# Performance work log

Hardware: AMD Instinct MI355X
Metric: run time of the kernel (lower is better)

## Reference

```python
import jax, jax.numpy as jnp
import numpy as np

B, N, C, D, E, VOC, T = 128, 49, 2048, 512, 512, 10000, 20


def setup_inputs() -> dict:
    key = jax.random.key(0)
    ks = jax.random.split(key, 24)
    rn = lambda k, s: (jax.random.normal(k, s) * 0.02).astype(jnp.float32)
    z = lambda s: jnp.zeros(s, dtype=jnp.float32)
    return {
        "image_feature": jax.random.normal(ks[0], (B, N, C), dtype=jnp.float32),
        "target": jax.random.randint(ks[1], (B, T), 0, VOC),
        "emb": rn(ks[2], (VOC, E)),
        "Wa": rn(ks[3], (D, C)), "ba": z((D,)),
        "Wb": rn(ks[4], (D, C)), "bb": z((D,)),
        "Whi": rn(ks[5], (D, C)), "bhi": z((D,)),
        "Wmi": rn(ks[6], (D, C)), "bmi": z((D,)),
        "Wih": rn(ks[7], (4 * D, D + E)), "bih": z((4 * D,)),
        "Whh": rn(ks[8], (4 * D, D)), "bhh": z((4 * D,)),
        "Wv": rn(ks[9], (N, D)),
        "Wg": rn(ks[10], (N, D)),
        "wh": rn(ks[11], (1, N)),
        "WH": rn(ks[12], (D, D)),
        "Wx": rn(ks[13], (D, D + E)),
        "Wh2": rn(ks[14], (D, D)),
        "Ws": rn(ks[15], (N, D)),
        "Wc": rn(ks[16], (D, D)), "bc": z((D,)),
        "Wfc": rn(ks[17], (D, D)), "bfc": z((D,)),
        "Wp": rn(ks[18], (VOC, D)), "bp": z((VOC,)),
    }


def _forward(image_feature, target, emb, Wa, ba, Wb, bb, Whi, bhi, Wmi, bmi,
             Wih, bih, Whh, bhh, Wv, Wg, wh, WH, Wx, Wh2, Ws, Wc, bc,
             Wfc, bfc, Wp, bp):
    relu, sig = jax.nn.relu, jax.nn.sigmoid
    Vf = relu(jnp.einsum('bnc,dc->bnd', image_feature, Wa) + ba)  # [B,N,D]
    mean = image_feature.mean(axis=1)                             # [B,C]
    vg = relu(mean @ Wb.T + bb)                                   # [B,D]
    h0 = relu(mean @ Whi.T + bhi)
    m0 = relu(mean @ Wmi.T + bmi)
    zbase = jnp.einsum('bnd,kd->bnk', Vf, Wv)                     # [B,N,N], fixed per image

    we = emb[target]                                              # [B,T,E]
    we = jnp.concatenate([jnp.zeros((we.shape[0], 1, we.shape[2]), we.dtype), we[:, :-1]], axis=1)
    we_t = jnp.swapaxes(we, 0, 1)                                 # [T,B,E]

    def step(carry, wemb):
        h, m = carry
        x = jnp.concatenate([vg, wemb], axis=1)                   # [B,D+E]
        hp = h
        gates = x @ Wih.T + bih + h @ Whh.T + bhh
        i, f, g, o = jnp.split(gates, 4, axis=1)
        m2 = sig(f) * m + sig(i) * jnp.tanh(g)
        h2 = sig(o) * jnp.tanh(m2)
        H = relu(h2 @ WH.T)                                       # [B,D]
        gH = H @ Wg.T                                             # [B,N]
        z = jnp.squeeze(jnp.tanh(zbase + gH[:, None, :]) @ wh.T, -1)  # [B,N]
        gt = sig(x @ Wx.T + hp @ Wh2.T)                           # [B,D]
        s = relu((gt * jnp.tanh(m2)) @ Wc.T + bc)                 # [B,D]
        z2 = jnp.tanh(s @ Ws.T + gH) @ wh.T                       # [B,1]
        alpha = jax.nn.softmax(jnp.concatenate([z, z2], axis=1), axis=1)  # [B,N+1]
        ctx = jnp.einsum('bn,bnd->bd', alpha[:, :-1], Vf) + alpha[:, -1:] * s
        out = jnp.tanh((H + ctx) @ Wfc.T + bfc)
        logit = out @ Wp.T + bp                                   # [B,VOC]
        return (h2, m2), (logit, alpha[:, :-1])

    _, (logits, attn) = jax.lax.scan(step, (h0, m0), we_t)
    logits = jnp.swapaxes(logits, 0, 1)                           # [B,T,VOC]
    attn = jnp.swapaxes(attn, 0, 1)                               # [B,T,N]
    return jax.nn.log_softmax(logits, axis=2), attn


def reference(image_feature, target, emb, Wa, ba, Wb, bb, Whi, bhi, Wmi, bmi,
              Wih, bih, Whh, bhh, Wv, Wg, wh, WH, Wx, Wh2, Ws, Wc, bc,
              Wfc, bfc, Wp, bp):
    return _forward(image_feature, target, emb, Wa, ba, Wb, bb, Whi, bhi,
                    Wmi, bmi, Wih, bih, Whh, bhh, Wv, Wg, wh, WH, Wx, Wh2,
                    Ws, Wc, bc, Wfc, bfc, Wp, bp)
```

## Files before the change

kernel.cpp:

```cpp
#include <hip/hip_runtime.h>
#include <hip/hip_bf16.h>

static const int kB = 128, kN = 49, kC = 2048, kD = 512, kE = 512, kV = 10000, kT = 20;

typedef __bf16 bf16x8 __attribute__((ext_vector_type(8)));
typedef float  f32x4v __attribute__((ext_vector_type(4)));
typedef _Float16 h8_t __attribute__((ext_vector_type(8)));
typedef _Float16 h2v_t __attribute__((ext_vector_type(2)));
typedef unsigned short u16;
typedef unsigned int u32;

#if defined(__has_builtin)
#if __has_builtin(__builtin_amdgcn_fdot2)
#define HAS_FDOT2 1
#endif
#endif
#ifndef HAS_FDOT2
#define HAS_FDOT2 0
#endif

#define AS1 __attribute__((address_space(1)))
#define AS3 __attribute__((address_space(3)))

__device__ __forceinline__ float sigmoidf_(float x){ return 1.f/(1.f+expf(-x)); }
__device__ __forceinline__ u16 f2b(float x){ __hip_bfloat16 h = __float2bfloat16(x); return *(u16*)&h; }
__device__ __forceinline__ float bu2f(u32 u){ u32 w = u << 16; union{u32 u; float f;} c; c.u = w; return c.f; }

#define TBM 128
#define TBN 128
#define TBK 32

__global__ __launch_bounds__(256) void gemm_bf16(
    const u16* __restrict__ A, int lda,
    const u16* __restrict__ W, int ldw,
    float* __restrict__ C, u16* __restrict__ Cbf, int ldc,
    int M, int N, int K,
    const float* __restrict__ bias,
    const float* __restrict__ add1, int ld1, int a1mask,
    int act,
    const u16* __restrict__ mul2, int ldm,
    int swz)
{
    __shared__ __align__(16) u16 As[TBM*TBK];
    __shared__ __align__(16) u16 Bs[TBN*TBK];
    const int tid = threadIdx.x;
    int bm, bn;
    if (swz){
        const int mblocks = (M + TBM - 1)/TBM;
        const int per_g = mblocks*8;
        const int id = blockIdx.x;
        const int g = id/per_g, r = id - g*per_g;
        bm = (r >> 3)*TBM;
        bn = (g*8 + (r & 7))*TBN;
        if (bn >= N) return;
    } else {
        bm = blockIdx.y * TBM;
        bn = blockIdx.x * TBN;
    }
    const int wave = tid >> 6, lane = tid & 63;
    const int wm = (wave >> 1) * 64, wn = (wave & 1) * 64;
    const int lm = lane & 15, quad = lane >> 4;
    f32x4v acc[4][4] = {};
    for (int k0 = 0; k0 < K; k0 += TBK) {
        #pragma unroll
        for (int h = 0; h < 2; ++h) {
            const int slot = h*256 + tid;
            const int row = slot >> 2, kf = (slot & 3)*8;
            const int wbase = (h*256 + (tid & 448))*8;
            __builtin_amdgcn_global_load_lds((const AS1 u32*)(A + (size_t)(bm + row)*lda + k0 + kf),
                                             (AS3 u32*)(As + wbase), 16, 0, 0);
            __builtin_amdgcn_global_load_lds((const AS1 u32*)(W + (size_t)(bn + row)*ldw + k0 + kf),
                                             (AS3 u32*)(Bs + wbase), 16, 0, 0);
        }
        __syncthreads();
        bf16x8 afr[4], bfr[4];
        #pragma unroll
        for (int i = 0; i < 4; ++i) afr[i] = *(const bf16x8*)&As[(wm + i*16 + lm)*TBK + quad*8];
        #pragma unroll
        for (int j = 0; j < 4; ++j) bfr[j] = *(const bf16x8*)&Bs[(wn + j*16 + lm)*TBK + quad*8];
        #pragma unroll
        for (int i = 0; i < 4; ++i)
            #pragma unroll
            for (int j = 0; j < 4; ++j)
                acc[i][j] = __builtin_amdgcn_mfma_f32_16x16x32_bf16(afr[i], bfr[j], acc[i][j], 0, 0, 0);
        __syncthreads();
    }
    #pragma unroll
    for (int i = 0; i < 4; ++i) {
        int mbase = bm + wm + i*16 + quad*4;
        #pragma unroll
        for (int j = 0; j < 4; ++j) {
            int n = bn + wn + j*16 + lm;
            if (n >= N) continue;
            float bv = bias ? bias[n] : 0.f;
            #pragma unroll
            for (int rr2 = 0; rr2 < 4; ++rr2) {
                int m = mbase + rr2;
                float v = acc[i][j][rr2] + bv;
                if (add1) v += add1[(size_t)(m & a1mask)*ld1 + n];
                if (act == 1) v = fmaxf(v, 0.f);
                else if (act == 2) v = tanhf(v);
                else if (act == 3) v = sigmoidf_(v) * bu2f(mul2[(size_t)m*ldm + n]);
                if (C)   C[(size_t)m*ldc + n] = v;
                if (Cbf) Cbf[(size_t)m*ldc + n] = f2b(v);
            }
        }
    }
}

__global__ __launch_bounds__(256) void img_cvt_mean_k(const float* __restrict__ img,
                                                      u16* __restrict__ img_bf,
                                                      u16* __restrict__ meanb){
    int idx = blockIdx.x*256 + threadIdx.x;
    int b = idx >> 8, c8 = idx & 255;
    const float* p = img + (size_t)b*kN*kC + c8*8;
    f32x4v s0 = {0,0,0,0}, s1 = {0,0,0,0};
    for (int n = 0; n < kN; ++n){
        f32x4v f0 = *(const f32x4v*)(p + (size_t)n*kC);
        f32x4v f1 = *(const f32x4v*)(p + (size_t)n*kC + 4);
        s0 += f0; s1 += f1;
        union { u16 u[8]; uint4 v; } pk;
        pk.u[0]=f2b(f0[0]); pk.u[1]=f2b(f0[1]); pk.u[2]=f2b(f0[2]); pk.u[3]=f2b(f0[3]);
        pk.u[4]=f2b(f1[0]); pk.u[5]=f2b(f1[1]); pk.u[6]=f2b(f1[2]); pk.u[7]=f2b(f1[3]);
        *(uint4*)(img_bf + ((size_t)(b*kN + n))*kC + c8*8) = pk.v;
    }
    const float inv = 1.f/(float)kN;
    union { u16 u[8]; uint4 v; } pm;
    pm.u[0]=f2b(s0[0]*inv); pm.u[1]=f2b(s0[1]*inv); pm.u[2]=f2b(s0[2]*inv); pm.u[3]=f2b(s0[3]*inv);
    pm.u[4]=f2b(s1[0]*inv); pm.u[5]=f2b(s1[1]*inv); pm.u[6]=f2b(s1[2]*inv); pm.u[7]=f2b(s1[3]*inv);
    *(uint4*)(meanb + (size_t)b*kC + c8*8) = pm.v;
}

struct CvtDesc {
    const float* src;
    unsigned long long dst;
    int src_ld, Kshift, mode, start;
};
struct CvtTab { CvtDesc d[17]; int total; };

__global__ __launch_bounds__(256) void multi_cvt_k(CvtTab tab){
    for (int idx = blockIdx.x*256 + threadIdx.x; idx < tab.total; idx += gridDim.x*256){
        int di = 0;
        #pragma unroll
        for (int i = 1; i < 17; ++i) if (idx >= tab.d[i].start) di = i;
        const CvtDesc D = tab.d[di];
        int rel = idx - D.start;
        int rr = rel >> D.Kshift, kc = rel - (rr << D.Kshift);
        const float* p = D.src + (size_t)rr*D.src_ld + kc*8;
        f32x4v f0 = *(const f32x4v*)p, f1 = *(const f32x4v*)(p+4);
        if (D.mode == 0){
            union { u16 u[8]; uint4 v; } pk;
            pk.u[0]=f2b(f0[0]); pk.u[1]=f2b(f0[1]); pk.u[2]=f2b(f0[2]); pk.u[3]=f2b(f0[3]);
            pk.u[4]=f2b(f1[0]); pk.u[5]=f2b(f1[1]); pk.u[6]=f2b(f1[2]); pk.u[7]=f2b(f1[3]);
            *(uint4*)((u16*)D.dst + (((size_t)rr << D.Kshift) + kc)*8) = pk.v;
        } else {
            h8_t o;
            o[0]=(_Float16)f0[0]; o[1]=(_Float16)f0[1]; o[2]=(_Float16)f0[2]; o[3]=(_Float16)f0[3];
            o[4]=(_Float16)f1[0]; o[5]=(_Float16)f1[1]; o[6]=(_Float16)f1[2]; o[7]=(_Float16)f1[3];
            *(h8_t*)((_Float16*)D.dst + ((size_t)kc*2048 + rr)*8) = o;
        }
    }
}

__global__ __launch_bounds__(256) void bias_prep_k(const float* bih, const float* bhh,
                                                   const float* bb, const float* bhi, const float* bmi,
                                                   float* bias2560, float* bcat3){
    int i = blockIdx.x*256 + threadIdx.x;
    if (i < 2048) bias2560[i] = bih[i] + bhh[i];
    else if (i < 2560) bias2560[i] = 0.f;
    else if (i < 4096){
        int j = i - 2560;
        bcat3[j] = (j < 512) ? bb[j] : (j < 1024 ? bhi[j-512] : bmi[j-1024]);
    }
}

__global__ __launch_bounds__(256) void emb_gather_k(const int* __restrict__ target,
                                                    const float* __restrict__ emb,
                                                    u16* __restrict__ we){
    int idx = blockIdx.x*256 + threadIdx.x;
    int e = idx & (kE-1);
    int rr = idx >> 9;
    int b = rr & 127, t = rr >> 7;
    float v = 0.f;
    if (t > 0){ int tok = target[b*kT + (t-1)]; v = emb[(size_t)tok*kE + e]; }
    we[idx] = f2b(v);
}

__global__ __launch_bounds__(256) void initcopy_k(const float* __restrict__ initC,
                                                  u16* __restrict__ hp_bf){
    int idx = blockIdx.x*256 + threadIdx.x;
    int b = idx >> 9, d = idx & 511;
    hp_bf[idx] = f2b(initC[(size_t)b*1536 + 512 + d]);
}

__device__ __forceinline__ float dot8f(h8_t a, h8_t b, float c){
#if HAS_FDOT2
    const h2v_t* ap = (const h2v_t*)&a;
    const h2v_t* bp = (const h2v_t*)&b;
    c = __builtin_amdgcn_fdot2(ap[0], bp[0], c, false);
    c = __builtin_amdgcn_fdot2(ap[1], bp[1], c, false);
    c = __builtin_amdgcn_fdot2(ap[2], bp[2], c, false);
    c = __builtin_amdgcn_fdot2(ap[3], bp[3], c, false);
#else
    #pragma unroll
    for (int i = 0; i < 8; ++i) c = fmaf((float)a[i], (float)b[i], c);
#endif
    return c;
}

__global__ __launch_bounds__(1024, 1) void scan_k(
    const float* __restrict__ initC,
    const float* __restrict__ xall,
    const _Float16* __restrict__ Wrec,
    u16* __restrict__ hp_bf,
    u16* __restrict__ tm_bf)
{
    const int b = blockIdx.x, tid = threadIdx.x;
    const int out = tid & 511, kh = tid >> 9;
    __shared__ __align__(16) _Float16 sh[512];
    __shared__ float spart[512][4];

    if (tid < 512) sh[tid] = (_Float16)initC[(size_t)b*1536 + 512 + tid];
    float m_reg = (kh == 0) ? initC[(size_t)b*1536 + 1024 + out] : 0.f;
    __syncthreads();

    for (int t = 0; t < kT; ++t){
        float a0=0.f, a1=0.f, a2=0.f, a3=0.f;
        const int kc0 = kh*32;
        #pragma unroll 2
        for (int kc = kc0; kc < kc0 + 32; ++kc){
            h8_t hv = *(const h8_t*)&sh[kc*8];
            const _Float16* wb = Wrec + (size_t)kc*2048*8;
            a0 = dot8f(hv, *(const h8_t*)&wb[(size_t)(out       )*8], a0);
            a1 = dot8f(hv, *(const h8_t*)&wb[(size_t)(out +  512)*8], a1);
            a2 = dot8f(hv, *(const h8_t*)&wb[(size_t)(out + 1024)*8], a2);
            a3 = dot8f(hv, *(const h8_t*)&wb[(size_t)(out + 1536)*8], a3);
        }
        __syncthreads();
        if (kh == 1){
            spart[out][0]=a0; spart[out][1]=a1; spart[out][2]=a2; spart[out][3]=a3;
        }
        __syncthreads();
        if (kh == 0){
            const float* xrow = xall + ((size_t)t*kB + b)*2560;
            a0 += spart[out][0] + xrow[out];
            a1 += spart[out][1] + xrow[out + 512];
            a2 += spart[out][2] + xrow[out + 1024];
            a3 += spart[out][3] + xrow[out + 1536];
            float i_g = sigmoidf_(a0), f_g = sigmoidf_(a1);
            float g_g = tanhf(a2),     o_g = sigmoidf_(a3);
            m_reg = f_g*m_reg + i_g*g_g;
            float tm = tanhf(m_reg);
            float h2 = o_g*tm;
            sh[out] = (_Float16)h2;
            hp_bf[((size_t)(t+1)*kB + b)*512 + out] = f2b(h2);
            tm_bf[((size_t)t*kB + b)*512 + out] = f2b(tm);
        }
        __syncthreads();
    }
}

__global__ __launch_bounds__(256) void attn_k(
    const float* __restrict__ H_all,
    const float* __restrict__ s_all,
    const u16* __restrict__ Wg_bf,
    const u16* __restrict__ Ws_bf,
    const u16* __restrict__ Vf_bf,
    const float* __restrict__ zbase,
    const float* __restrict__ wh,
    u16* __restrict__ Hc_bf,
    float* __restrict__ attn_out)
{
    const int r = blockIdx.x, tid = threadIdx.x;
    const int b = r & 127, t = r >> 7;
    __shared__ float sH2[512], ss2[512];
    __shared__ float sgH[52], ssWs[52], swh[52], sz[52], salpha[52];

    for (int d = tid; d < 512; d += 256){
        sH2[d] = H_all[(size_t)r*512 + d];
        ss2[d] = s_all[(size_t)r*512 + d];
    }
    if (tid < 49) swh[tid] = wh[tid];
    __syncthreads();
    if (tid < 49){
        const u16* wr = Wg_bf + (size_t)tid*512;
        float a = 0.f;
        for (int k = 0; k < 512; k += 8){
            uint4 v = *(const uint4*)(wr + k);
            a += bu2f(v.x&0xffff)*sH2[k]   + bu2f(v.x>>16)*sH2[k+1]
               + bu2f(v.y&0xffff)*sH2[k+2] + bu2f(v.y>>16)*sH2[k+3]
               + bu2f(v.z&0xffff)*sH2[k+4] + bu2f(v.z>>16)*sH2[k+5]
               + bu2f(v.w&0xffff)*sH2[k+6] + bu2f(v.w>>16)*sH2[k+7];
        }
        sgH[tid] = a;
    } else if (tid >= 64 && tid < 113){
        int n = tid - 64;
        const u16* wr = Ws_bf + (size_t)n*512;
        float a = 0.f;
        for (int k = 0; k < 512; k += 8){
            uint4 v = *(const uint4*)(wr + k);
            a += bu2f(v.x&0xffff)*ss2[k]   + bu2f(v.x>>16)*ss2[k+1]
               + bu2f(v.y&0xffff)*ss2[k+2] + bu2f(v.y>>16)*ss2[k+3]
               + bu2f(v.z&0xffff)*ss2[k+4] + bu2f(v.z>>16)*ss2[k+5]
               + bu2f(v.w&0xffff)*ss2[k+6] + bu2f(v.w>>16)*ss2[k+7];
        }
        ssWs[n] = a;
    }
    __syncthreads();
    if (tid < 49){
        const float* zb = zbase + (size_t)b*2401 + (size_t)tid*49;
        float a = 0.f;
        #pragma unroll
        for (int k = 0; k < 49; ++k) a += tanhf(zb[k] + sgH[k]) * swh[k];
        sz[tid] = a;
    } else if (tid == 64){
        float a = 0.f;
        #pragma unroll
        for (int k = 0; k < 49; ++k) a += tanhf(ssWs[k] + sgH[k]) * swh[k];
        sz[49] = a;
    }
    __syncthreads();
    if (tid < 64){
        float val = (tid < 50) ? sz[tid] : -1e30f;
        float mx = val;
        #pragma unroll
        for (int o = 32; o > 0; o >>= 1) mx = fmaxf(mx, __shfl_xor(mx, o));
        float e = (tid < 50) ? __expf(val - mx) : 0.f;
        float ssum = e;
        #pragma unroll
        for (int o = 32; o > 0; o >>= 1) ssum += __shfl_xor(ssum, o);
        float a = e/ssum;
        if (tid < 50) salpha[tid] = a;
        if (tid < 49) attn_out[((size_t)b*kT + t)*kN + tid] = a;
    }
    __syncthreads();
    for (int d = tid; d < 512; d += 256){
        float a = salpha[49] * ss2[d];
        const u16* vf = Vf_bf + (size_t)b*49*512 + d;
        #pragma unroll
        for (int n = 0; n < 49; ++n) a = fmaf(salpha[n], bu2f(vf[(size_t)n*512]), a);
        Hc_bf[(size_t)r*512 + d] = f2b(sH2[d] + a);
    }
}

__global__ __launch_bounds__(256) void logsoftmax_k(const u16* __restrict__ logits_bf,
                                                    float* __restrict__ out0)
{
    const int r = blockIdx.x, tid = threadIdx.x;
    const int b = r / 20, t = r - b*20;
    const u16* L = logits_bf + (size_t)(t*kB + b)*kV;
    __shared__ float rm[256], rs[256];
    float m = -1e30f, s = 0.f;
    for (int c = tid; c < kV/8; c += 256){
        uint4 v = *(const uint4*)(L + c*8);
        u32 w[4] = {v.x, v.y, v.z, v.w};
        #pragma unroll
        for (int j = 0; j < 4; ++j){
            float x0 = bu2f(w[j] & 0xffff), x1 = bu2f(w[j] >> 16);
            float nm = fmaxf(m, fmaxf(x0, x1));
            s = s*__expf(m - nm) + __expf(x0 - nm) + __expf(x1 - nm);
            m = nm;
        }
    }
    rm[tid] = m; rs[tid] = s; __syncthreads();
    for (int st = 128; st > 0; st >>= 1){
        if (tid < st){
            float m2 = rm[tid + st], s2 = rs[tid + st];
            float nm = fmaxf(rm[tid], m2);
            rs[tid] = rs[tid]*__expf(rm[tid] - nm) + s2*__expf(m2 - nm);
            rm[tid] = nm;
        }
        __syncthreads();
    }
    float lse = rm[0] + logf(rs[0]);
    float* D = out0 + (size_t)r*kV;
    for (int c = tid; c < kV/8; c += 256){
        uint4 v = *(const uint4*)(L + c*8);
        u32 w[4] = {v.x, v.y, v.z, v.w};
        f32x4v o0, o1;
        o0[0]=bu2f(w[0]&0xffff)-lse; o0[1]=bu2f(w[0]>>16)-lse;
        o0[2]=bu2f(w[1]&0xffff)-lse; o0[3]=bu2f(w[1]>>16)-lse;
        o1[0]=bu2f(w[2]&0xffff)-lse; o1[1]=bu2f(w[2]>>16)-lse;
        o1[2]=bu2f(w[3]&0xffff)-lse; o1[3]=bu2f(w[3]>>16)-lse;
        *(f32x4v*)(D + c*8) = o0;
        *(f32x4v*)(D + c*8 + 4) = o1;
    }
}

extern "C" void kernel_launch(void* const* d_in, const int* in_sizes, int n_in,
                              void* d_out, int out_size, void* d_ws, size_t ws_size,
                              hipStream_t stream)
{
    const float* img   = (const float*)d_in[0];
    const int*   target= (const int*)  d_in[1];
    const float* emb   = (const float*)d_in[2];
    const float* Wa    = (const float*)d_in[3];
    const float* ba    = (const float*)d_in[4];
    const float* Wb    = (const float*)d_in[5];
    const float* bb    = (const float*)d_in[6];
    const float* Whi   = (const float*)d_in[7];
    const float* bhi   = (const float*)d_in[8];
    const float* Wmi   = (const float*)d_in[9];
    const float* bmi   = (const float*)d_in[10];
    const float* Wih   = (const float*)d_in[11];
    const float* bih   = (const float*)d_in[12];
    const float* Whh   = (const float*)d_in[13];
    const float* bhh   = (const float*)d_in[14];
    const float* Wv    = (const float*)d_in[15];
    const float* Wg    = (const float*)d_in[16];
    const float* wh    = (const float*)d_in[17];
    const float* W_H   = (const float*)d_in[18];
    const float* Wx    = (const float*)d_in[19];
    const float* Wh2   = (const float*)d_in[20];
    const float* Wsm   = (const float*)d_in[21];
    const float* Wc    = (const float*)d_in[22];
    const float* bc    = (const float*)d_in[23];
    const float* Wfc   = (const float*)d_in[24];
    const float* bfc   = (const float*)d_in[25];
    const float* Wp    = (const float*)d_in[26];
    const float* bp    = (const float*)d_in[27];
    (void)in_sizes; (void)n_in; (void)out_size; (void)ws_size;

    float* out0 = (float*)d_out;
    float* attn_out = out0 + (size_t)kB*kT*kV;

    char* base = (char*)d_ws;
    size_t off = 0;
    auto alloc = [&](size_t bytes)->char*{
        char* p = base + off;
        off += ((bytes + 255) & ~(size_t)255);
        return p;
    };
    u16* Wa_bf     = (u16*)alloc((size_t)kD*kC*2);
    u16* Winit_bf  = (u16*)alloc((size_t)1536*kC*2);
    u16* Wv_bf     = (u16*)alloc((size_t)128*kD*2);
    u16* Wp_bf     = (u16*)alloc((size_t)10112*kD*2);
    u16* Wfirst_bf = (u16*)alloc((size_t)2560*512*2);
    u16* Wlast_bf  = (u16*)alloc((size_t)2560*512*2);
    _Float16* Wrec4 = (_Float16*)alloc((size_t)2048*512*2);
    u16* Wh2_bf    = (u16*)alloc((size_t)512*512*2);
    u16* WH_bf     = (u16*)alloc((size_t)512*512*2);
    u16* Wc_bf     = (u16*)alloc((size_t)512*512*2);
    u16* Wg_bf     = (u16*)alloc((size_t)128*512*2);
    u16* Ws_bf     = (u16*)alloc((size_t)128*512*2);
    u16* Wfc_bf    = (u16*)alloc((size_t)512*512*2);
    float* bias2560 = (float*)alloc(2560*4);
    float* bcat3    = (float*)alloc(1536*4);
    u16* meanb_bf   = (u16*)alloc((size_t)kB*kC*2);
    float* initC    = (float*)alloc((size_t)kB*1536*4);
    u16* init_bf    = (u16*)alloc((size_t)kB*1536*2);
    u16* Vf_bf      = (u16*)alloc((size_t)kB*kN*kD*2);
    float* zbase    = (float*)alloc((size_t)kB*kN*kN*4);
    u16* we_bf      = (u16*)alloc((size_t)kT*kB*kE*2);
    float* gbase    = (float*)alloc((size_t)kB*2560*4);
    u16* outbf      = (u16*)alloc((size_t)kT*kB*kD*2);
    u16* gtv_bf     = (u16*)alloc((size_t)kT*kB*kD*2);
    u16* hp_bf      = (u16*)alloc((size_t)(kT+1)*kB*kD*2);
    u16* tm_bf      = (u16*)alloc((size_t)kT*kB*kD*2);

    char* dyn = base + off;
    u16* img_bf    = (u16*)dyn;
    float* xall    = (float*)(dyn + (((size_t)kB*kN*kC*2 + 255) & ~(size_t)255));
    u16* logits_bf = (u16*)dyn;
    size_t poff = 0;
    auto palloc = [&](size_t bytes)->char*{
        char* p = dyn + poff;
        poff += ((bytes + 255) & ~(size_t)255);
        return p;
    };
    float* H_all   = (float*)palloc((size_t)kT*kB*kD*4);
    float* s_all   = (float*)palloc((size_t)kT*kB*kD*4);
    u16*   Hc_bf   = (u16*)  palloc((size_t)kT*kB*kD*2);

    auto G = [&](const u16* A, int lda, const u16* W, int ldw,
                 float* C, u16* Cbf, int ldc, int M, int N, int K,
                 const float* bias, const float* a1, int l1, int a1mask, int act,
                 const u16* mul2 = nullptr, int ldm = 0){
        dim3 g((N + TBN - 1)/TBN, (M + TBM - 1)/TBM);
        gemm_bf16<<<g, 256, 0, stream>>>(A, lda, W, ldw, C, Cbf, ldc, M, N, K,
                                         bias, a1, l1, a1mask, act, mul2, ldm, 0);
    };

    bias_prep_k<<<16, 256, 0, stream>>>(bih, bhh, bb, bhi, bmi, bias2560, bcat3);
    emb_gather_k<<<kT*kB*kE/256, 256, 0, stream>>>(target, emb, we_bf);
    img_cvt_mean_k<<<kB*kC/8/256, 256, 0, stream>>>(img, img_bf, meanb_bf);
    {
        CvtTab tab{};
        int idx = 0, start = 0;
        auto add = [&](const float* src, void* dst, int src_ld, int Kshift, int rows, int mode){
            tab.d[idx] = {src, (unsigned long long)(size_t)dst, src_ld, Kshift, mode, start};
            start += rows << Kshift; ++idx;
        };
        add(Wa,        Wa_bf,                        2048, 8, 512,   0);
        add(Wb,        Winit_bf,                     2048, 8, 512,   0);
        add(Whi,       Winit_bf + (size_t)512*kC,    2048, 8, 512,   0);
        add(Wmi,       Winit_bf + (size_t)1024*kC,   2048, 8, 512,   0);
        add(Wv,        Wv_bf,                         512, 6, 49,    0);
        add(Wp,        Wp_bf,                         512, 6, 10000, 0);
        add(Wih,       Wfirst_bf,                    1024, 6, 2048,  0);
        add(Wx,        Wfirst_bf + (size_t)2048*512, 1024, 6, 512,   0);
        add(Wih + 512, Wlast_bf,                     1024, 6, 2048,  0);
        add(Wx  + 512, Wlast_bf + (size_t)2048*512,  1024, 6, 512,   0);
        add(W_H,       WH_bf,                         512, 6, 512,   0);
        add(Wc,        Wc_bf,                         512, 6, 512,   0);
        add(Wg,        Wg_bf,                         512, 6, 49,    0);
        add(Wsm,       Ws_bf,                         512, 6, 49,    0);
        add(Wfc,       Wfc_bf,                        512, 6, 512,   0);
        add(Whh,       Wrec4,                         512, 6, 2048,  5);
        add(Wh2,       Wh2_bf,                        512, 6, 512,   0);
        tab.total = start;
        int blocks = (start + 255)/256; if (blocks > 2048) blocks = 2048;
        multi_cvt_k<<<blocks, 256, 0, stream>>>(tab);
    }

    G(meanb_bf, kC, Winit_bf, kC, initC, init_bf, 1536, kB, 1536, kC, bcat3, nullptr, 0, -1, 1);
    initcopy_k<<<kB*kD/256, 256, 0, stream>>>(initC, hp_bf);
    G(img_bf, kC, Wa_bf, kC, nullptr, Vf_bf, kD, kB*kN, kD, kC, ba, nullptr, 0, -1, 1);
    G(Vf_bf, kD, Wv_bf, kD, zbase, nullptr, kN, kB*kN, kN, kD, nullptr, nullptr, 0, -1, 0);
    G(init_bf, 1536, Wfirst_bf, 512, gbase, nullptr, 2560, kB, 2560, kD, bias2560, nullptr, 0, -1, 0);
    G(we_bf, kE, Wlast_bf, 512, xall, nullptr, 2560, kT*kB, 2560, kE, nullptr, gbase, 2560, 127, 0);

    scan_k<<<kB, 1024, 0, stream>>>(initC, xall, Wrec4, hp_bf, tm_bf);

    G(hp_bf, kD, Wh2_bf, kD, nullptr, gtv_bf, kD, kT*kB, kD, kD,
      nullptr, xall + 2048, 2560, 0x7fffffff, 3, tm_bf, kD);
    G(hp_bf + (size_t)kB*kD, kD, WH_bf, kD, H_all, nullptr, kD, kT*kB, kD, kD, nullptr, nullptr, 0, -1, 1);
    G(gtv_bf, kD, Wc_bf, kD, s_all, nullptr, kD, kT*kB, kD, kD, bc, nullptr, 0, -1, 1);
    attn_k<<<kT*kB, 256, 0, stream>>>(H_all, s_all, Wg_bf, Ws_bf, Vf_bf, zbase, wh,
                                      Hc_bf, attn_out);
    G(Hc_bf, kD, Wfc_bf, kD, nullptr, outbf, kD, kT*kB, kD, kD, bfc, nullptr, 0, -1, 2);

    {
        const int mblocks = (kT*kB + TBM - 1)/TBM;
        const int nblocks = (kV + TBN - 1)/TBN;
        const int groups  = (nblocks + 7)/8;
        dim3 g(groups*8*mblocks, 1);
        gemm_bf16<<<g, 256, 0, stream>>>(outbf, kD, Wp_bf, kD, nullptr, logits_bf, kV,
                                         kT*kB, kV, kD, bp, nullptr, 0, -1, 0, nullptr, 0, 1);
    }
    logsoftmax_k<<<kB*kT, 256, 0, stream>>>(logits_bf, out0);
}
```

Measured before the change: 1.039 ms.

## Quantize recurrent LSTM weights to FP8, deepen GEMM K tile, remap attention blocks

The recurrent Whh weights are now stored as FP8 with per-row scales and dequantized inside the sequential scan kernel, halving the weight bytes streamed every timestep. The hidden state is kept in fp32 shared memory. The GEMM K tile is doubled from 32 to 64, issuing two MFMA sub-steps per barrier pair to cut synchronization overhead. The attention kernel's block-to-(t,b) mapping is permuted so blocks of the same batch element land on the same XCD. FP8 weights lower recurrent precision and may push error toward tolerance, and the larger tile doubles LDS use per block.

```diff
diff --git a/kernel.cpp b/kernel.cpp
--- a/kernel.cpp
+++ b/kernel.cpp
@@ -5,18 +5,19 @@
 
 typedef __bf16 bf16x8 __attribute__((ext_vector_type(8)));
 typedef float  f32x4v __attribute__((ext_vector_type(4)));
+typedef float  f32x2v __attribute__((ext_vector_type(2)));
 typedef _Float16 h8_t __attribute__((ext_vector_type(8)));
-typedef _Float16 h2v_t __attribute__((ext_vector_type(2)));
 typedef unsigned short u16;
 typedef unsigned int u32;
+typedef unsigned char u8;
 
 #if defined(__has_builtin)
-#if __has_builtin(__builtin_amdgcn_fdot2)
-#define HAS_FDOT2 1
+#if __has_builtin(__builtin_amdgcn_cvt_pk_f32_fp8) && __has_builtin(__builtin_amdgcn_cvt_pk_fp8_f32)
+#define HAS_FP8CVT 1
 #endif
 #endif
-#ifndef HAS_FDOT2
-#define HAS_FDOT2 0
+#ifndef HAS_FP8CVT
+#define HAS_FP8CVT 0
 #endif
 
 #define AS1 __attribute__((address_space(1)))
@@ -26,9 +27,57 @@
 __device__ __forceinline__ u16 f2b(float x){ __hip_bfloat16 h = __float2bfloat16(x); return *(u16*)&h; }
 __device__ __forceinline__ float bu2f(u32 u){ u32 w = u << 16; union{u32 u; float f;} c; c.u = w; return c.f; }
 
+#if !HAS_FP8CVT
+__device__ __forceinline__ float dec_fp8(u8 b){
+    int s = b >> 7, e = (b >> 3) & 15, m = b & 7;
+    float v = e ? ldexpf(1.f + m*0.125f, e - 7) : ldexpf(m*0.125f, -6);
+    return s ? -v : v;
+}
+__device__ __forceinline__ u8 enc_fp8(float v){
+    u8 s = (v < 0.f) ? 0x80 : 0;
+    float a = fabsf(v);
+    if (!(a > 0.f)) return 0;
+    a = fminf(a, 448.f);
+    int e; float fr = frexpf(a, &e);
+    (void)fr;
+    int ebits = e - 1 + 7;
+    if (ebits < 1){
+        float q = rintf(ldexpf(a, 9));
+        if (q >= 8.f) return s | 0x08;
+        return s | (u8)(int)q;
+    }
+    float mant = ldexpf(a, -(e - 1));
+    int m = (int)rintf((mant - 1.f)*8.f);
+    if (m == 8){ m = 0; ebits++; }
+    if (ebits > 15){ ebits = 15; m = 6; }
+    return s | (u8)(ebits << 3) | (u8)m;
+}
+#endif
+
+__device__ __forceinline__ float dot8_fp8(uint2 w, f32x4v ha, f32x4v hb, float c){
+#if HAS_FP8CVT
+    f32x2v d0 = __builtin_amdgcn_cvt_pk_f32_fp8((int)w.x, false);
+    f32x2v d1 = __builtin_amdgcn_cvt_pk_f32_fp8((int)w.x, true);
+    f32x2v d2 = __builtin_amdgcn_cvt_pk_f32_fp8((int)w.y, false);
+    f32x2v d3 = __builtin_amdgcn_cvt_pk_f32_fp8((int)w.y, true);
+    c = fmaf(d0[0], ha[0], c); c = fmaf(d0[1], ha[1], c);
+    c = fmaf(d1[0], ha[2], c); c = fmaf(d1[1], ha[3], c);
+    c = fmaf(d2[0], hb[0], c); c = fmaf(d2[1], hb[1], c);
+    c = fmaf(d3[0], hb[2], c); c = fmaf(d3[1], hb[3], c);
+#else
+    u8 by[8];
+    *(u32*)&by[0] = w.x; *(u32*)&by[4] = w.y;
+    c = fmaf(dec_fp8(by[0]), ha[0], c); c = fmaf(dec_fp8(by[1]), ha[1], c);
+    c = fmaf(dec_fp8(by[2]), ha[2], c); c = fmaf(dec_fp8(by[3]), ha[3], c);
+    c = fmaf(dec_fp8(by[4]), hb[0], c); c = fmaf(dec_fp8(by[5]), hb[1], c);
+    c = fmaf(dec_fp8(by[6]), hb[2], c); c = fmaf(dec_fp8(by[7]), hb[3], c);
+#endif
+    return c;
+}
+
 #define TBM 128
 #define TBN 128
-#define TBK 32
+#define TBK 64
 
 __global__ __launch_bounds__(256) void gemm_bf16(
     const u16* __restrict__ A, int lda,
@@ -63,26 +112,29 @@
     f32x4v acc[4][4] = {};
     for (int k0 = 0; k0 < K; k0 += TBK) {
         #pragma unroll
-        for (int h = 0; h < 2; ++h) {
+        for (int h = 0; h < 4; ++h) {
             const int slot = h*256 + tid;
-            const int row = slot >> 2, kf = (slot & 3)*8;
-            const int wbase = (h*256 + (tid & 448))*8;
+            const int row = slot >> 3, kf = (slot & 7)*8;
+            const int wbase = (h*256 + (tid & 192))*8;
             __builtin_amdgcn_global_load_lds((const AS1 u32*)(A + (size_t)(bm + row)*lda + k0 + kf),
                                              (AS3 u32*)(As + wbase), 16, 0, 0);
             __builtin_amdgcn_global_load_lds((const AS1 u32*)(W + (size_t)(bn + row)*ldw + k0 + kf),
                                              (AS3 u32*)(Bs + wbase), 16, 0, 0);
         }
         __syncthreads();
-        bf16x8 afr[4], bfr[4];
-        #pragma unroll
-        for (int i = 0; i < 4; ++i) afr[i] = *(const bf16x8*)&As[(wm + i*16 + lm)*TBK + quad*8];
-        #pragma unroll
-        for (int j = 0; j < 4; ++j) bfr[j] = *(const bf16x8*)&Bs[(wn + j*16 + lm)*TBK + quad*8];
-        #pragma unroll
-        for (int i = 0; i < 4; ++i)
+        #pragma unroll
+        for (int sub = 0; sub < 2; ++sub){
+            bf16x8 afr[4], bfr[4];
             #pragma unroll
-            for (int j = 0; j < 4; ++j)
-                acc[i][j] = __builtin_amdgcn_mfma_f32_16x16x32_bf16(afr[i], bfr[j], acc[i][j], 0, 0, 0);
+            for (int i = 0; i < 4; ++i) afr[i] = *(const bf16x8*)&As[(wm + i*16 + lm)*TBK + quad*8 + sub*32];
+            #pragma unroll
+            for (int j = 0; j < 4; ++j) bfr[j] = *(const bf16x8*)&Bs[(wn + j*16 + lm)*TBK + quad*8 + sub*32];
+            #pragma unroll
+            for (int i = 0; i < 4; ++i)
+                #pragma unroll
+                for (int j = 0; j < 4; ++j)
+                    acc[i][j] = __builtin_amdgcn_mfma_f32_16x16x32_bf16(afr[i], bfr[j], acc[i][j], 0, 0, 0);
+        }
         __syncthreads();
     }
     #pragma unroll
@@ -134,32 +186,54 @@
 struct CvtDesc {
     const float* src;
     unsigned long long dst;
-    int src_ld, Kshift, mode, start;
+    int src_ld, Kshift, start;
 };
-struct CvtTab { CvtDesc d[17]; int total; };
+struct CvtTab { CvtDesc d[16]; int total; };
 
 __global__ __launch_bounds__(256) void multi_cvt_k(CvtTab tab){
     for (int idx = blockIdx.x*256 + threadIdx.x; idx < tab.total; idx += gridDim.x*256){
         int di = 0;
         #pragma unroll
-        for (int i = 1; i < 17; ++i) if (idx >= tab.d[i].start) di = i;
+        for (int i = 1; i < 16; ++i) if (idx >= tab.d[i].start) di = i;
         const CvtDesc D = tab.d[di];
         int rel = idx - D.start;
         int rr = rel >> D.Kshift, kc = rel - (rr << D.Kshift);
         const float* p = D.src + (size_t)rr*D.src_ld + kc*8;
         f32x4v f0 = *(const f32x4v*)p, f1 = *(const f32x4v*)(p+4);
-        if (D.mode == 0){
-            union { u16 u[8]; uint4 v; } pk;
-            pk.u[0]=f2b(f0[0]); pk.u[1]=f2b(f0[1]); pk.u[2]=f2b(f0[2]); pk.u[3]=f2b(f0[3]);
-            pk.u[4]=f2b(f1[0]); pk.u[5]=f2b(f1[1]); pk.u[6]=f2b(f1[2]); pk.u[7]=f2b(f1[3]);
-            *(uint4*)((u16*)D.dst + (((size_t)rr << D.Kshift) + kc)*8) = pk.v;
-        } else {
-            h8_t o;
-            o[0]=(_Float16)f0[0]; o[1]=(_Float16)f0[1]; o[2]=(_Float16)f0[2]; o[3]=(_Float16)f0[3];
-            o[4]=(_Float16)f1[0]; o[5]=(_Float16)f1[1]; o[6]=(_Float16)f1[2]; o[7]=(_Float16)f1[3];
-            *(h8_t*)((_Float16*)D.dst + ((size_t)kc*2048 + rr)*8) = o;
-        }
-    }
+        union { u16 u[8]; uint4 v; } pk;
+        pk.u[0]=f2b(f0[0]); pk.u[1]=f2b(f0[1]); pk.u[2]=f2b(f0[2]); pk.u[3]=f2b(f0[3]);
+        pk.u[4]=f2b(f1[0]); pk.u[5]=f2b(f1[1]); pk.u[6]=f2b(f1[2]); pk.u[7]=f2b(f1[3]);
+        *(uint4*)((u16*)D.dst + (((size_t)rr << D.Kshift) + kc)*8) = pk.v;
+    }
+}
+
+__global__ __launch_bounds__(512) void wrec8_prep_k(const float* __restrict__ Whh,
+                                                    u8* __restrict__ W8,
+                                                    float* __restrict__ rowscale){
+    const int row = (blockIdx.x << 3) + (threadIdx.x >> 6);
+    const int l = threadIdx.x & 63;
+    const float* src = Whh + (size_t)row*512 + l*8;
+    f32x4v v0 = *(const f32x4v*)src, v1 = *(const f32x4v*)(src + 4);
+    float mx = 0.f;
+    #pragma unroll
+    for (int i = 0; i < 4; ++i){ mx = fmaxf(mx, fabsf(v0[i])); mx = fmaxf(mx, fabsf(v1[i])); }
+    #pragma unroll
+    for (int o = 32; o > 0; o >>= 1) mx = fmaxf(mx, __shfl_xor(mx, o));
+    const float se = (mx > 0.f) ? 448.f/mx : 0.f;
+    if (l == 0) rowscale[row] = (mx > 0.f) ? mx/448.f : 0.f;
+    u32 lo, hi;
+#if HAS_FP8CVT
+    lo = (u32)__builtin_amdgcn_cvt_pk_fp8_f32(v0[0]*se, v0[1]*se, 0, false);
+    lo = (u32)__builtin_amdgcn_cvt_pk_fp8_f32(v0[2]*se, v0[3]*se, (int)lo, true);
+    hi = (u32)__builtin_amdgcn_cvt_pk_fp8_f32(v1[0]*se, v1[1]*se, 0, false);
+    hi = (u32)__builtin_amdgcn_cvt_pk_fp8_f32(v1[2]*se, v1[3]*se, (int)hi, true);
+#else
+    u8 by[8];
+    #pragma unroll
+    for (int i = 0; i < 4; ++i){ by[i] = enc_fp8(v0[i]*se); by[4+i] = enc_fp8(v1[i]*se); }
+    lo = *(u32*)&by[0]; hi = *(u32*)&by[4];
+#endif
+    *(uint2*)&W8[((size_t)l*2048 + row)*8] = make_uint2(lo, hi);
 }
 
 __global__ __launch_bounds__(256) void bias_prep_k(const float* bih, const float* bhh,
@@ -193,35 +267,23 @@
     hp_bf[idx] = f2b(initC[(size_t)b*1536 + 512 + d]);
 }
 
-__device__ __forceinline__ float dot8f(h8_t a, h8_t b, float c){
-#if HAS_FDOT2
-    const h2v_t* ap = (const h2v_t*)&a;
-    const h2v_t* bp = (const h2v_t*)&b;
-    c = __builtin_amdgcn_fdot2(ap[0], bp[0], c, false);
-    c = __builtin_amdgcn_fdot2(ap[1], bp[1], c, false);
-    c = __builtin_amdgcn_fdot2(ap[2], bp[2], c, false);
-    c = __builtin_amdgcn_fdot2(ap[3], bp[3], c, false);
-#else
-    #pragma unroll
-    for (int i = 0; i < 8; ++i) c = fmaf((float)a[i], (float)b[i], c);
-#endif
-    return c;
-}
-
 __global__ __launch_bounds__(1024, 1) void scan_k(
     const float* __restrict__ initC,
     const float* __restrict__ xall,
-    const _Float16* __restrict__ Wrec,
+    const u8* __restrict__ Wrec8,
+    const float* __restrict__ rowscale,
     u16* __restrict__ hp_bf,
     u16* __restrict__ tm_bf)
 {
     const int b = blockIdx.x, tid = threadIdx.x;
     const int out = tid & 511, kh = tid >> 9;
-    __shared__ __align__(16) _Float16 sh[512];
+    __shared__ __align__(16) float shf[512];
     __shared__ float spart[512][4];
 
-    if (tid < 512) sh[tid] = (_Float16)initC[(size_t)b*1536 + 512 + tid];
+    if (tid < 512) shf[tid] = initC[(size_t)b*1536 + 512 + tid];
     float m_reg = (kh == 0) ? initC[(size_t)b*1536 + 1024 + out] : 0.f;
+    const float rs0 = rowscale[out],        rs1 = rowscale[512 + out];
+    const float rs2 = rowscale[1024 + out], rs3 = rowscale[1536 + out];
     __syncthreads();
 
     for (int t = 0; t < kT; ++t){
@@ -229,12 +291,17 @@
         const int kc0 = kh*32;
         #pragma unroll 2
         for (int kc = kc0; kc < kc0 + 32; ++kc){
-            h8_t hv = *(const h8_t*)&sh[kc*8];
-            const _Float16* wb = Wrec + (size_t)kc*2048*8;
-            a0 = dot8f(hv, *(const h8_t*)&wb[(size_t)(out       )*8], a0);
-            a1 = dot8f(hv, *(const h8_t*)&wb[(size_t)(out +  512)*8], a1);
-            a2 = dot8f(hv, *(const h8_t*)&wb[(size_t)(out + 1024)*8], a2);
-            a3 = dot8f(hv, *(const h8_t*)&wb[(size_t)(out + 1536)*8], a3);
+            const u8* wb = Wrec8 + ((size_t)kc*2048 + out)*8;
+            f32x4v ha = *(const f32x4v*)&shf[kc*8];
+            f32x4v hb = *(const f32x4v*)&shf[kc*8 + 4];
+            uint2 w0 = *(const uint2*)(wb);
+            uint2 w1 = *(const uint2*)(wb + 4096);
+            uint2 w2 = *(const uint2*)(wb + 8192);
+            uint2 w3 = *(const uint2*)(wb + 12288);
+            a0 = dot8_fp8(w0, ha, hb, a0);
+            a1 = dot8_fp8(w1, ha, hb, a1);
+            a2 = dot8_fp8(w2, ha, hb, a2);
+            a3 = dot8_fp8(w3, ha, hb, a3);
         }
         __syncthreads();
         if (kh == 1){
@@ -243,16 +310,16 @@
         __syncthreads();
         if (kh == 0){
             const float* xrow = xall + ((size_t)t*kB + b)*2560;
-            a0 += spart[out][0] + xrow[out];
-            a1 += spart[out][1] + xrow[out + 512];
-            a2 += spart[out][2] + xrow[out + 1024];
-            a3 += spart[out][3] + xrow[out + 1536];
+            a0 = (a0 + spart[out][0])*rs0 + xrow[out];
+            a1 = (a1 + spart[out][1])*rs1 + xrow[out + 512];
+            a2 = (a2 + spart[out][2])*rs2 + xrow[out + 1024];
+            a3 = (a3 + spart[out][3])*rs3 + xrow[out + 1536];
             float i_g = sigmoidf_(a0), f_g = sigmoidf_(a1);
             float g_g = tanhf(a2),     o_g = sigmoidf_(a3);
             m_reg = f_g*m_reg + i_g*g_g;
             float tm = tanhf(m_reg);
             float h2 = o_g*tm;
-            sh[out] = (_Float16)h2;
+            shf[out] = h2;
             hp_bf[((size_t)(t+1)*kB + b)*512 + out] = f2b(h2);
             tm_bf[((size_t)t*kB + b)*512 + out] = f2b(tm);
         }
@@ -271,8 +338,10 @@
     u16* __restrict__ Hc_bf,
     float* __restrict__ attn_out)
 {
-    const int r = blockIdx.x, tid = threadIdx.x;
-    const int b = r & 127, t = r >> 7;
+    const int id = blockIdx.x, tid = threadIdx.x;
+    const int xcd = id & 7, q = id >> 3;
+    const int t = q % 20, b = xcd + 8*(q/20);
+    const int r = t*128 + b;
     __shared__ float sH2[512], ss2[512];
     __shared__ float sgH[52], ssWs[52], swh[52], sz[52], salpha[52];
 
@@ -437,7 +506,8 @@
     u16* Wp_bf     = (u16*)alloc((size_t)10112*kD*2);
     u16* Wfirst_bf = (u16*)alloc((size_t)2560*512*2);
     u16* Wlast_bf  = (u16*)alloc((size_t)2560*512*2);
-    _Float16* Wrec4 = (_Float16*)alloc((size_t)2048*512*2);
+    u8*  Wrec8     = (u8*)alloc((size_t)64*2048*8);
+    float* rowscale = (float*)alloc(2048*4);
     u16* Wh2_bf    = (u16*)alloc((size_t)512*512*2);
     u16* WH_bf     = (u16*)alloc((size_t)512*512*2);
     u16* Wc_bf     = (u16*)alloc((size_t)512*512*2);
@@ -484,30 +554,30 @@
     bias_prep_k<<<16, 256, 0, stream>>>(bih, bhh, bb, bhi, bmi, bias2560, bcat3);
     emb_gather_k<<<kT*kB*kE/256, 256, 0, stream>>>(target, emb, we_bf);
     img_cvt_mean_k<<<kB*kC/8/256, 256, 0, stream>>>(img, img_bf, meanb_bf);
+    wrec8_prep_k<<<256, 512, 0, stream>>>(Whh, Wrec8, rowscale);
     {
         CvtTab tab{};
         int idx = 0, start = 0;
-        auto add = [&](const float* src, void* dst, int src_ld, int Kshift, int rows, int mode){
-            tab.d[idx] = {src, (unsigned long long)(size_t)dst, src_ld, Kshift, mode, start};
+        auto add = [&](const float* src, void* dst, int src_ld, int Kshift, int rows){
+            tab.d[idx] = {src, (unsigned long long)(size_t)dst, src_ld, Kshift, start};
             start += rows << Kshift; ++idx;
         };
-        add(Wa,        Wa_bf,                        2048, 8, 512,   0);
-        add(Wb,        Winit_bf,                     2048, 8, 512,   0);
-        add(Whi,       Winit_bf + (size_t)512*kC,    2048, 8, 512,   0);
-        add(Wmi,       Winit_bf + (size_t)1024*kC,   2048, 8, 512,   0);
-        add(Wv,        Wv_bf,                         512, 6, 49,    0);
-        add(Wp,        Wp_bf,                         512, 6, 10000, 0);
-        add(Wih,       Wfirst_bf,                    1024, 6, 2048,  0);
-        add(Wx,        Wfirst_bf + (size_t)2048*512, 1024, 6, 512,   0);
-        add(Wih + 512, Wlast_bf,                     1024, 6, 2048,  0);
-        add(Wx  + 512, Wlast_bf + (size_t)2048*512,  1024, 6, 512,   0);
-        add(W_H,       WH_bf,                         512, 6, 512,   0);
-        add(Wc,        Wc_bf,                         512, 6, 512,   0);
-        add(Wg,        Wg_bf,                         512, 6, 49,    0);
-        add(Wsm,       Ws_bf,                         512, 6, 49,    0);
-        add(Wfc,       Wfc_bf,                        512, 6, 512,   0);
-        add(Whh,       Wrec4,                         512, 6, 2048,  5);
-        add(Wh2,       Wh2_bf,                        512, 6, 512,   0);
+        add(Wa,        Wa_bf,                        2048, 8, 512);
+        add(Wb,        Winit_bf,                     2048, 8, 512);
+        add(Whi,       Winit_bf + (size_t)512*kC,    2048, 8, 512);
+        add(Wmi,       Winit_bf + (size_t)1024*kC,   2048, 8, 512);
+        add(Wv,        Wv_bf,                         512, 6, 49);
+        add(Wp,        Wp_bf,                         512, 6, 10000);
+        add(Wih,       Wfirst_bf,                    1024, 6, 2048);
+        add(Wx,        Wfirst_bf + (size_t)2048*512, 1024, 6, 512);
+        add(Wih + 512, Wlast_bf,                     1024, 6, 2048);
+        add(Wx  + 512, Wlast_bf + (size_t)2048*512,  1024, 6, 512);
+        add(W_H,       WH_bf,                         512, 6, 512);
+        add(Wc,        Wc_bf,                         512, 6, 512);
+        add(Wg,        Wg_bf,                         512, 6, 49);
+        add(Wsm,       Ws_bf,                         512, 6, 49);
+        add(Wfc,       Wfc_bf,                        512, 6, 512);
+        add(Wh2,       Wh2_bf,                        512, 6, 512);
         tab.total = start;
         int blocks = (start + 255)/256; if (blocks > 2048) blocks = 2048;
         multi_cvt_k<<<blocks, 256, 0, stream>>>(tab);
@@ -520,7 +590,7 @@
     G(init_bf, 1536, Wfirst_bf, 512, gbase, nullptr, 2560, kB, 2560, kD, bias2560, nullptr, 0, -1, 0);
     G(we_bf, kE, Wlast_bf, 512, xall, nullptr, 2560, kT*kB, 2560, kE, nullptr, gbase, 2560, 127, 0);
 
-    scan_k<<<kB, 1024, 0, stream>>>(initC, xall, Wrec4, hp_bf, tm_bf);
+    scan_k<<<kB, 1024, 0, stream>>>(initC, xall, Wrec8, rowscale, hp_bf, tm_bf);
 
     G(hp_bf, kD, Wh2_bf, kD, nullptr, gtv_bf, kD, kT*kB, kD, kD,
       nullptr, xall + 2048, 2560, 0x7fffffff, 3, tm_bf, kD);
```

New measurement: 1.096 ms. 5.5% more time.
